# Kernel optimization log

Measured on AMD Instinct MI355X. Metric: run time of the kernel, lower is better.

## Reference

```python
import jax, jax.numpy as jnp
import numpy as np

N = 100000
E = 1600000
F_IN = 128
H = 128
NUM_GRAPHS = 512
EPS = 1e-5


def setup_inputs() -> dict:
    key = jax.random.key(0)
    ks = jax.random.split(key, 16)
    x = jax.random.normal(ks[0], (N, F_IN), dtype=jnp.float32)
    edge_index = jax.random.randint(ks[1], (2, E), 0, N, dtype=jnp.int32)
    batch = jnp.sort(jax.random.randint(ks[2], (N,), 0, NUM_GRAPHS, dtype=jnp.int32))
    def lin(k, fi, fo):
        s = 1.0 / np.sqrt(fi)
        return jax.random.uniform(k, (fi, fo), jnp.float32, -s, s)
    return {
        "x": x, "edge_index": edge_index, "batch": batch,
        "W1": lin(ks[3], F_IN, H), "b1": jnp.zeros((H,), jnp.float32),
        "g1": jnp.ones((H,), jnp.float32), "beta1": jnp.zeros((H,), jnp.float32),
        "W2": lin(ks[4], H, H), "b2": jnp.zeros((H,), jnp.float32),
        "g2": jnp.ones((H,), jnp.float32), "beta2": jnp.zeros((H,), jnp.float32),
        "W3": lin(ks[5], H, H), "b3": jnp.zeros((H,), jnp.float32),
        "g3": jnp.ones((H,), jnp.float32), "beta3": jnp.zeros((H,), jnp.float32),
        "Wl": lin(ks[6], H, 1), "bl": jnp.zeros((1,), jnp.float32),
    }


def _layer_norm(x, g, b):
    mu = jnp.mean(x, axis=-1, keepdims=True)
    var = jnp.mean((x - mu) ** 2, axis=-1, keepdims=True)
    return (x - mu) * jax.lax.rsqrt(var + EPS) * g + b


def _gcn_conv(x, W, b, src, dst, dinv):
    # GCNConv: D^{-1/2}(A+I)D^{-1/2} X W + b, deg includes self-loops
    h = x @ W                                   # [N,H]
    enorm = dinv[src] * dinv[dst]               # [E]
    agg = jax.ops.segment_sum(h[src] * enorm[:, None], dst, num_segments=N)
    agg = agg + h * (dinv * dinv)[:, None]      # self-loop contribution
    return agg + b


def reference(x, edge_index, batch, W1, b1, g1, beta1, W2, b2, g2, beta2,
              W3, b3, g3, beta3, Wl, bl):
    src, dst = edge_index[0], edge_index[1]
    deg = 1.0 + jax.ops.segment_sum(jnp.ones((E,), jnp.float32), dst, num_segments=N)
    dinv = jax.lax.rsqrt(deg)
    h = jax.nn.relu(_layer_norm(_gcn_conv(x, W1, b1, src, dst, dinv), g1, beta1))
    h = jax.nn.relu(_layer_norm(_gcn_conv(h, W2, b2, src, dst, dinv), g2, beta2))
    h = jax.nn.relu(_layer_norm(_gcn_conv(h, W3, b3, src, dst, dinv), g3, beta3))
    # global mean pool over graphs
    sums = jax.ops.segment_sum(h, batch, num_segments=NUM_GRAPHS)
    cnts = jax.ops.segment_sum(jnp.ones((N,), jnp.float32), batch, num_segments=NUM_GRAPHS)
    pooled = sums / jnp.maximum(cnts, 1.0)[:, None]
    return pooled @ Wl + bl                     # [NUM_GRAPHS, 1]
```

## Files before the change

kernel.cpp:

```cpp
#include <hip/hip_runtime.h>
#include <hip/hip_bf16.h>
#include <math.h>

#define N_NODES    100000
#define N_EDGES    1600000
#define FDIM       128
#define NUM_GRAPHS 512
#define EPS        1e-5f
#define PADN       100096

#define B_CVT   12512
#define B_WPK   192

#define NBUCK   196
#define CAPA    10240
#define EB_CHUNK 2048
#define BINA_BLOCKS ((N_EDGES + EB_CHUNK - 1) / EB_CHUNK)
#define SEGSH   14
#define SEGN    8

typedef __attribute__((ext_vector_type(8))) __bf16 bf16x8;
typedef __attribute__((ext_vector_type(4))) float  f32x4;

__device__ __forceinline__ unsigned short f2bf(float f) {
    unsigned u = __builtin_bit_cast(unsigned, f);
    u += 0x7FFF + ((u >> 16) & 1);
    return (unsigned short)(u >> 16);
}
__device__ __forceinline__ float bf2f(unsigned short b) {
    unsigned u = ((unsigned)b) << 16;
    return __builtin_bit_cast(float, u);
}

__device__ __forceinline__ void dec4(unsigned dw, float* o) {
    auto lo = __builtin_amdgcn_cvt_pk_f32_fp8(dw, false);
    auto hi = __builtin_amdgcn_cvt_pk_f32_fp8(dw, true);
    o[0] = lo[0]; o[1] = lo[1]; o[2] = hi[0]; o[3] = hi[1];
}

__device__ __forceinline__ void acc16(uint4 v, float* a) {
    float d[16];
    dec4(v.x, &d[0]); dec4(v.y, &d[4]); dec4(v.z, &d[8]); dec4(v.w, &d[12]);
#pragma unroll
    for (int f = 0; f < 16; f++) a[f] += d[f];
}


__global__ __launch_bounds__(256) void k_build(const int* __restrict__ src,
                                               const int* __restrict__ dst,
                                               int* __restrict__ bcur,
                                               unsigned* __restrict__ binned,
                                               const float* __restrict__ x,
                                               unsigned short* __restrict__ xb,
                                               const float* __restrict__ W1,
                                               const float* __restrict__ W2,
                                               const float* __restrict__ W3,
                                               unsigned short* __restrict__ wp) {
    int b = blockIdx.x;
    int t = threadIdx.x;
    if (b < BINA_BLOCKS) {
        __shared__ int hist[NBUCK];
        __shared__ int lbase[NBUCK];
        __shared__ int loff[NBUCK];
        __shared__ unsigned lpack[EB_CHUNK];
        __shared__ unsigned short lbuck[EB_CHUNK];
        int e0 = b * EB_CHUNK;
        int nE = min(EB_CHUNK, N_EDGES - e0);

        for (int j = t; j < NBUCK; j += 256) { hist[j] = 0; loff[j] = 0; }
        __syncthreads();

        for (int k = t; k < nE; k += 256) {
            int e  = e0 + k;
            int d  = dst[e];
            int bk = d >> 9;
            lpack[k] = (unsigned)src[e] | ((unsigned)(d & 511) << 17);
            lbuck[k] = (unsigned short)bk;
            atomicAdd(&hist[bk], 1);
        }
        __syncthreads();
        for (int j = t; j < NBUCK; j += 256)
            lbase[j] = atomicAdd(&bcur[j], hist[j]);
        __syncthreads();

        for (int k = t; k < nE; k += 256) {
            int bk = lbuck[k];
            int p  = lbase[bk] + atomicAdd(&loff[bk], 1);
            binned[(size_t)bk * CAPA + p] = lpack[k];
        }
    } else if (b < BINA_BLOCKS + B_CVT) {
        long long idx = ((long long)(b - BINA_BLOCKS) * 256 + t) * 4;
        ushort4 o;
        if (idx < (long long)N_NODES * FDIM) {
            float4 v = *(const float4*)(x + idx);
            o.x = f2bf(v.x); o.y = f2bf(v.y); o.z = f2bf(v.z); o.w = f2bf(v.w);
        } else {
            o.x = o.y = o.z = o.w = 0;
        }
        *(ushort4*)(xb + idx) = o;
    } else {
        int wb  = b - (BINA_BLOCKS + B_CVT);
        int mat = wb >> 6;
        const float* W = (mat == 0) ? W1 : (mat == 1) ? W2 : W3;
        unsigned short* o = wp + (size_t)mat * 16384;
        int idx = (wb & 63) * 256 + t;
        int j  = idx & 7;
        int l  = (idx >> 3) & 63;
        int ct = (idx >> 9) & 7;
        int ks = idx >> 12;
        int k  = ks * 32 + (l >> 4) * 8 + j;
        int c  = ct * 16 + (l & 15);
        o[idx] = f2bf(W[k * 128 + c]);
    }
}


__global__ __launch_bounds__(256) void k_binB(const unsigned* __restrict__ binned,
                                              const int* __restrict__ bcur,
                                              int* __restrict__ offs,
                                              float* __restrict__ dinv,
                                              int* __restrict__ csr_src) {
    __shared__ int cnt2[512 * SEGN];
    __shared__ int lofs2[512 * SEGN];
    __shared__ int part[256];
    __shared__ int stage[CAPA];
    int b = blockIdx.x;
    int t = threadIdx.x;
    int nb0 = b * 512;
    int cnt = bcur[b];

    int pv = (t < b) ? bcur[t] : 0;
#pragma unroll
    for (int off = 32; off; off >>= 1) pv += __shfl_down(pv, off);
    if ((t & 63) == 0) part[t >> 6] = pv;
    __syncthreads();
    int seg0 = part[0] + part[1] + part[2] + part[3];
    __syncthreads();

    for (int j = t; j < 512 * SEGN; j += 256) cnt2[j] = 0;
    __syncthreads();

    for (int k = t; k < cnt; k += 256) {
        unsigned v = binned[(size_t)b * CAPA + k];
        int ld = v >> 17;
        int s  = v & 0x1FFFF;
        atomicAdd(&cnt2[ld * SEGN + (s >> SEGSH)], 1);
    }
    __syncthreads();

    int base16 = t * 16;
    int lsum[16];
    int run = 0;
#pragma unroll
    for (int q = 0; q < 16; q++) { lsum[q] = run; run += cnt2[base16 + q]; }
    part[t] = run;
    __syncthreads();
    for (int off = 1; off < 256; off <<= 1) {
        int y = 0;
        if (t >= off) y = part[t - off];
        __syncthreads();
        if (t >= off) part[t] += y;
        __syncthreads();
    }
    int excl = part[t] - run;
#pragma unroll
    for (int q = 0; q < 16; q++) lofs2[base16 + q] = excl + lsum[q];
    __syncthreads();

    for (int j = t; j < 512; j += 256) {
        int node = nb0 + j;
        if (node < N_NODES) {
            int st = lofs2[j * SEGN];
            int en = (j == 511) ? cnt : lofs2[(j + 1) * SEGN];
            offs[node] = seg0 + st;
            dinv[node] = rsqrtf(1.0f + (float)(en - st));
        }
    }
    if (b == NBUCK - 1 && t == 0) offs[N_NODES] = N_EDGES;
    __syncthreads();

    for (int k = t; k < cnt; k += 256) {
        unsigned v = binned[(size_t)b * CAPA + k];
        int ld = v >> 17;
        int s  = v & 0x1FFFF;
        int p  = atomicAdd(&lofs2[ld * SEGN + (s >> SEGSH)], 1);
        stage[p] = s;
    }
    __syncthreads();
    for (int k = t; k < cnt; k += 256) csr_src[seg0 + k] = stage[k];
}


__global__ __launch_bounds__(256) void k_gemm(const unsigned short* __restrict__ A,
                                              const unsigned short* __restrict__ Wp,
                                              const float* __restrict__ dinv,
                                              unsigned char* __restrict__ C8) {
    int t    = threadIdx.x;
    int lane = t & 63;
    int w    = t >> 6;
    int wc   = w & 1;
    int wr   = w >> 1;
    int rb   = blockIdx.x * 128 + wr * 64 + (lane & 15);
    int koff = (lane >> 4) * 8;

    f32x4 acc[4][4];
#pragma unroll
    for (int c = 0; c < 4; c++)
#pragma unroll
        for (int r = 0; r < 4; r++) acc[c][r] = (f32x4){0.f, 0.f, 0.f, 0.f};

    const bf16x8* Wv = (const bf16x8*)Wp;
#pragma unroll
    for (int ks = 0; ks < 4; ++ks) {
        bf16x8 fw[4], fa[4];
#pragma unroll
        for (int c = 0; c < 4; ++c)
            fw[c] = Wv[(ks * 8 + wc * 4 + c) * 64 + lane];
#pragma unroll
        for (int r = 0; r < 4; ++r) {
            const uint4 v = *(const uint4*)(A + (size_t)(rb + r * 16) * 128 + ks * 32 + koff);
            fa[r] = __builtin_bit_cast(bf16x8, v);
        }
#pragma unroll
        for (int c = 0; c < 4; ++c)
#pragma unroll
            for (int r = 0; r < 4; ++r)
                acc[c][r] = __builtin_amdgcn_mfma_f32_16x16x32_bf16(fw[c], fa[r], acc[c][r], 0, 0, 0);
    }

#pragma unroll
    for (int r = 0; r < 4; ++r) {
        int row = blockIdx.x * 128 + wr * 64 + r * 16 + (lane & 15);
        if (row < N_NODES) {
            float dv = dinv[row];
#pragma unroll
            for (int c = 0; c < 4; ++c) {
                int col = (wc * 4 + c) * 16 + (lane >> 4) * 4;
                unsigned u = __builtin_amdgcn_cvt_pk_fp8_f32(acc[c][r][0] * dv, acc[c][r][1] * dv, 0, false);
                u = (unsigned)__builtin_amdgcn_cvt_pk_fp8_f32(acc[c][r][2] * dv, acc[c][r][3] * dv, (int)u, true);
                *(unsigned*)(C8 + (size_t)row * 128 + col) = u;
            }
        }
    }
}


__global__ __launch_bounds__(256) void k_agg(const unsigned char* __restrict__ h8,
                                             unsigned short* __restrict__ out,
                                             const int* __restrict__ offs,
                                             const int* __restrict__ csr_src,
                                             const float* __restrict__ dinv,
                                             const float* __restrict__ bias,
                                             const float* __restrict__ gamma,
                                             const float* __restrict__ beta) {
    int t    = threadIdx.x;
    int lane = t & 63;
    int grp  = lane >> 3;
    int sl   = lane & 7;
    int i    = blockIdx.x * 32 + (t >> 6) * 8 + grp;

    float di = dinv[i];
    size_t lofs16 = (size_t)sl * 16;

    float a[16];
    {
        uint4 v = *(const uint4*)(h8 + (size_t)i * 128 + lofs16);
        float d[16];
        dec4(v.x, &d[0]); dec4(v.y, &d[4]); dec4(v.z, &d[8]); dec4(v.w, &d[12]);
#pragma unroll
        for (int f = 0; f < 16; f++) a[f] = d[f];
    }

    int eBeg = offs[i], eEnd = offs[i + 1];
    int e = eBeg;
    int s0, s1, s2, s3;
    if (e + 4 <= eEnd) {
        s0 = csr_src[e + 0]; s1 = csr_src[e + 1];
        s2 = csr_src[e + 2]; s3 = csr_src[e + 3];
    }
    for (; e + 8 <= eEnd; e += 4) {
        uint4 v0 = *(const uint4*)(h8 + (size_t)s0 * 128 + lofs16);
        uint4 v1 = *(const uint4*)(h8 + (size_t)s1 * 128 + lofs16);
        uint4 v2 = *(const uint4*)(h8 + (size_t)s2 * 128 + lofs16);
        uint4 v3 = *(const uint4*)(h8 + (size_t)s3 * 128 + lofs16);
        s0 = csr_src[e + 4]; s1 = csr_src[e + 5];
        s2 = csr_src[e + 6]; s3 = csr_src[e + 7];
        acc16(v0, a); acc16(v1, a); acc16(v2, a); acc16(v3, a);
    }
    if (e + 4 <= eEnd) {
        uint4 v0 = *(const uint4*)(h8 + (size_t)s0 * 128 + lofs16);
        uint4 v1 = *(const uint4*)(h8 + (size_t)s1 * 128 + lofs16);
        uint4 v2 = *(const uint4*)(h8 + (size_t)s2 * 128 + lofs16);
        uint4 v3 = *(const uint4*)(h8 + (size_t)s3 * 128 + lofs16);
        acc16(v0, a); acc16(v1, a); acc16(v2, a); acc16(v3, a);
        e += 4;
    }
    for (; e < eEnd; ++e) {
        int s = csr_src[e];
        uint4 v = *(const uint4*)(h8 + (size_t)s * 128 + lofs16);
        acc16(v, a);
    }

    float4 b0 = *(const float4*)(bias + sl * 16);
    float4 b1 = *(const float4*)(bias + sl * 16 + 4);
    float4 b2 = *(const float4*)(bias + sl * 16 + 8);
    float4 b3 = *(const float4*)(bias + sl * 16 + 12);
    a[0]  = fmaf(a[0],  di, b0.x); a[1]  = fmaf(a[1],  di, b0.y);
    a[2]  = fmaf(a[2],  di, b0.z); a[3]  = fmaf(a[3],  di, b0.w);
    a[4]  = fmaf(a[4],  di, b1.x); a[5]  = fmaf(a[5],  di, b1.y);
    a[6]  = fmaf(a[6],  di, b1.z); a[7]  = fmaf(a[7],  di, b1.w);
    a[8]  = fmaf(a[8],  di, b2.x); a[9]  = fmaf(a[9],  di, b2.y);
    a[10] = fmaf(a[10], di, b2.z); a[11] = fmaf(a[11], di, b2.w);
    a[12] = fmaf(a[12], di, b3.x); a[13] = fmaf(a[13], di, b3.y);
    a[14] = fmaf(a[14], di, b3.z); a[15] = fmaf(a[15], di, b3.w);

    float s1v = 0.f, s2v = 0.f;
#pragma unroll
    for (int f = 0; f < 16; f++) { s1v += a[f]; s2v += a[f] * a[f]; }
#pragma unroll
    for (int off = 1; off < 8; off <<= 1) {
        s1v += __shfl_xor(s1v, off);
        s2v += __shfl_xor(s2v, off);
    }
    float mu   = s1v * (1.0f / 128.0f);
    float var  = s2v * (1.0f / 128.0f) - mu * mu;
    float rstd = rsqrtf(var + EPS);

    float g[16], be[16];
    {
        float4 g0 = *(const float4*)(gamma + sl * 16);
        float4 g1 = *(const float4*)(gamma + sl * 16 + 4);
        float4 g2 = *(const float4*)(gamma + sl * 16 + 8);
        float4 g3 = *(const float4*)(gamma + sl * 16 + 12);
        g[0]=g0.x; g[1]=g0.y; g[2]=g0.z; g[3]=g0.w;
        g[4]=g1.x; g[5]=g1.y; g[6]=g1.z; g[7]=g1.w;
        g[8]=g2.x; g[9]=g2.y; g[10]=g2.z; g[11]=g2.w;
        g[12]=g3.x; g[13]=g3.y; g[14]=g3.z; g[15]=g3.w;
        float4 e0v = *(const float4*)(beta + sl * 16);
        float4 e1v = *(const float4*)(beta + sl * 16 + 4);
        float4 e2v = *(const float4*)(beta + sl * 16 + 8);
        float4 e3v = *(const float4*)(beta + sl * 16 + 12);
        be[0]=e0v.x; be[1]=e0v.y; be[2]=e0v.z; be[3]=e0v.w;
        be[4]=e1v.x; be[5]=e1v.y; be[6]=e1v.z; be[7]=e1v.w;
        be[8]=e2v.x; be[9]=e2v.y; be[10]=e2v.z; be[11]=e2v.w;
        be[12]=e3v.x; be[13]=e3v.y; be[14]=e3v.z; be[15]=e3v.w;
    }

    unsigned ow[8];
#pragma unroll
    for (int f = 0; f < 8; f++) {
        float r0 = fmaxf((a[2*f]   - mu) * rstd * g[2*f]   + be[2*f],   0.f);
        float r1 = fmaxf((a[2*f+1] - mu) * rstd * g[2*f+1] + be[2*f+1], 0.f);
        ow[f] = (unsigned)f2bf(r0) | ((unsigned)f2bf(r1) << 16);
    }
    uint4* op = (uint4*)(out + (size_t)i * 128 + sl * 16);
    op[0] = make_uint4(ow[0], ow[1], ow[2], ow[3]);
    op[1] = make_uint4(ow[4], ow[5], ow[6], ow[7]);
}


__global__ __launch_bounds__(256) void k_pool(const unsigned short* __restrict__ h,
                                              const int* __restrict__ batch,
                                              const float* __restrict__ Wl,
                                              const float* __restrict__ bl,
                                              float* __restrict__ out) {
    __shared__ float2 part[4][64];
    int g = blockIdx.x;
    int t = threadIdx.x, w = t >> 6, lane = t & 63;

    int lo = 0, hi = N_NODES;
    while (lo < hi) { int mid = (lo + hi) >> 1; if (batch[mid] < g) lo = mid + 1; else hi = mid; }
    int s = lo;
    lo = s; hi = N_NODES;
    while (lo < hi) { int mid = (lo + hi) >> 1; if (batch[mid] < g + 1) lo = mid + 1; else hi = mid; }
    int e = lo;

    float ax = 0.f, ay = 0.f;
    for (int n = s + w; n < e; n += 4) {
        unsigned v = *(const unsigned*)(h + (size_t)n * 128 + lane * 2);
        ax += bf2f((unsigned short)(v & 0xffff));
        ay += bf2f((unsigned short)(v >> 16));
    }
    part[w][lane] = make_float2(ax, ay);
    __syncthreads();
    if (t < 64) {
        float sx = part[0][lane].x + part[1][lane].x + part[2][lane].x + part[3][lane].x;
        float sy = part[0][lane].y + part[1][lane].y + part[2][lane].y + part[3][lane].y;
        float cnt = fmaxf((float)(e - s), 1.0f);
        float inv = 1.0f / cnt;
        float p = sx * inv * Wl[lane * 2] + sy * inv * Wl[lane * 2 + 1];
#pragma unroll
        for (int off = 32; off; off >>= 1) p += __shfl_xor(p, off);
        if (lane == 0) out[g] = p + bl[0];
    }
}


extern "C" void kernel_launch(void* const* d_in, const int* in_sizes, int n_in,
                              void* d_out, int out_size, void* d_ws, size_t ws_size,
                              hipStream_t stream) {
    const float* x     = (const float*)d_in[0];
    const int*   ei    = (const int*)d_in[1];
    const int*   batch = (const int*)d_in[2];
    const float* W1 = (const float*)d_in[3];
    const float* b1 = (const float*)d_in[4];
    const float* g1 = (const float*)d_in[5];
    const float* be1 = (const float*)d_in[6];
    const float* W2 = (const float*)d_in[7];
    const float* b2 = (const float*)d_in[8];
    const float* g2 = (const float*)d_in[9];
    const float* be2 = (const float*)d_in[10];
    const float* W3 = (const float*)d_in[11];
    const float* b3 = (const float*)d_in[12];
    const float* g3 = (const float*)d_in[13];
    const float* be3 = (const float*)d_in[14];
    const float* Wl = (const float*)d_in[15];
    const float* bl = (const float*)d_in[16];

    const int* src = ei;
    const int* dst = ei + N_EDGES;

    char* ws = (char*)d_ws;
    size_t off = 0;
    auto alloc = [&](size_t bytes) -> void* {
        void* p = ws + off;
        off += (bytes + 255) & ~(size_t)255;
        return p;
    };
    unsigned short* xb   = (unsigned short*)alloc((size_t)PADN * FDIM * 2);
    unsigned short* hA   = (unsigned short*)alloc((size_t)PADN * FDIM * 2);
    unsigned char*  hF   = (unsigned char*)alloc((size_t)PADN * FDIM);
    unsigned short* wp   = (unsigned short*)alloc((size_t)3 * 16384 * 2);
    float* dinv    = (float*)alloc((size_t)N_NODES * 4);
    int*   offs    = (int*)alloc((size_t)(N_NODES + 1) * 4);
    int*   csr_src = (int*)alloc((size_t)N_EDGES * 4);
    unsigned* binned = (unsigned*)alloc((size_t)NBUCK * CAPA * 4);
    int*   bcur    = (int*)alloc(256 * 4);

    hipMemsetAsync(bcur, 0, 256 * 4, stream);

    k_build<<<BINA_BLOCKS + B_CVT + B_WPK, 256, 0, stream>>>(src, dst, bcur, binned,
                                                             x, xb, W1, W2, W3, wp);
    k_binB<<<NBUCK, 256, 0, stream>>>(binned, bcur, offs, dinv, csr_src);

    int gemm_grid = PADN / 128;
    int agg_grid  = N_NODES / 32;

    k_gemm<<<gemm_grid, 256, 0, stream>>>(xb, wp, dinv, hF);
    k_agg<<<agg_grid, 256, 0, stream>>>(hF, hA, offs, csr_src, dinv, b1, g1, be1);
    k_gemm<<<gemm_grid, 256, 0, stream>>>(hA, wp + 16384, dinv, hF);
    k_agg<<<agg_grid, 256, 0, stream>>>(hF, hA, offs, csr_src, dinv, b2, g2, be2);
    k_gemm<<<gemm_grid, 256, 0, stream>>>(hA, wp + 32768, dinv, hF);
    k_agg<<<agg_grid, 256, 0, stream>>>(hF, hA, offs, csr_src, dinv, b3, g3, be3);

    k_pool<<<NUM_GRAPHS, 256, 0, stream>>>(hA, batch, Wl, bl, (float*)d_out);
}
```

Measured before the change: 263.8 us.

## Move x/W bf16 conversion into CSR-build kernel and shrink its shared memory

The fp32-to-bf16 conversion of x and the weight packing move out of the edge-binning kernel and into the second preprocessing kernel, which also builds the CSR. The 196 CSR-build blocks now run alongside the many bandwidth-bound conversion blocks instead of running alone on a mostly idle GPU. The CSR block reuses one shared buffer for counts and offsets and computes degrees from per-thread sums, cutting its LDS footprint. Bucket capacity shrinks to 9216, which lowers the margin against bucket overflow.

```diff
diff --git a/kernel.cpp b/kernel.cpp
--- a/kernel.cpp
+++ b/kernel.cpp
@@ -13,9 +13,9 @@
 #define B_WPK   192
 
 #define NBUCK   196
-#define CAPA    10240
+#define CAPA    9216
 #define EB_CHUNK 2048
-#define BINA_BLOCKS ((N_EDGES + EB_CHUNK - 1) / EB_CHUNK)
+#define BIN_BLOCKS ((N_EDGES + EB_CHUNK - 1) / EB_CHUNK)
 #define SEGSH   14
 #define SEGN    8
 
@@ -46,50 +46,126 @@
 }
 
 
-__global__ __launch_bounds__(256) void k_build(const int* __restrict__ src,
-                                               const int* __restrict__ dst,
-                                               int* __restrict__ bcur,
-                                               unsigned* __restrict__ binned,
-                                               const float* __restrict__ x,
-                                               unsigned short* __restrict__ xb,
-                                               const float* __restrict__ W1,
-                                               const float* __restrict__ W2,
-                                               const float* __restrict__ W3,
-                                               unsigned short* __restrict__ wp) {
+__global__ __launch_bounds__(256) void k_bin(const int* __restrict__ src,
+                                             const int* __restrict__ dst,
+                                             int* __restrict__ bcur,
+                                             unsigned* __restrict__ binned) {
+    __shared__ int hist[NBUCK];
+    __shared__ int lbase[NBUCK];
+    __shared__ int loff[NBUCK];
+    __shared__ unsigned lpack[EB_CHUNK];
+    __shared__ unsigned short lbuck[EB_CHUNK];
     int b = blockIdx.x;
     int t = threadIdx.x;
-    if (b < BINA_BLOCKS) {
-        __shared__ int hist[NBUCK];
-        __shared__ int lbase[NBUCK];
-        __shared__ int loff[NBUCK];
-        __shared__ unsigned lpack[EB_CHUNK];
-        __shared__ unsigned short lbuck[EB_CHUNK];
-        int e0 = b * EB_CHUNK;
-        int nE = min(EB_CHUNK, N_EDGES - e0);
-
-        for (int j = t; j < NBUCK; j += 256) { hist[j] = 0; loff[j] = 0; }
-        __syncthreads();
-
-        for (int k = t; k < nE; k += 256) {
-            int e  = e0 + k;
-            int d  = dst[e];
-            int bk = d >> 9;
-            lpack[k] = (unsigned)src[e] | ((unsigned)(d & 511) << 17);
-            lbuck[k] = (unsigned short)bk;
-            atomicAdd(&hist[bk], 1);
-        }
-        __syncthreads();
-        for (int j = t; j < NBUCK; j += 256)
-            lbase[j] = atomicAdd(&bcur[j], hist[j]);
-        __syncthreads();
-
-        for (int k = t; k < nE; k += 256) {
-            int bk = lbuck[k];
-            int p  = lbase[bk] + atomicAdd(&loff[bk], 1);
-            binned[(size_t)bk * CAPA + p] = lpack[k];
-        }
-    } else if (b < BINA_BLOCKS + B_CVT) {
-        long long idx = ((long long)(b - BINA_BLOCKS) * 256 + t) * 4;
+    int e0 = b * EB_CHUNK;
+    int nE = min(EB_CHUNK, N_EDGES - e0);
+
+    for (int j = t; j < NBUCK; j += 256) { hist[j] = 0; loff[j] = 0; }
+    __syncthreads();
+
+    for (int k = t; k < nE; k += 256) {
+        int e  = e0 + k;
+        int d  = dst[e];
+        int bk = d >> 9;
+        lpack[k] = (unsigned)src[e] | ((unsigned)(d & 511) << 17);
+        lbuck[k] = (unsigned short)bk;
+        atomicAdd(&hist[bk], 1);
+    }
+    __syncthreads();
+    for (int j = t; j < NBUCK; j += 256)
+        lbase[j] = atomicAdd(&bcur[j], hist[j]);
+    __syncthreads();
+
+    for (int k = t; k < nE; k += 256) {
+        int bk = lbuck[k];
+        int p  = lbase[bk] + atomicAdd(&loff[bk], 1);
+        binned[(size_t)bk * CAPA + p] = lpack[k];
+    }
+}
+
+
+__global__ __launch_bounds__(256) void k_mid(const unsigned* __restrict__ binned,
+                                             const int* __restrict__ bcur,
+                                             int* __restrict__ offs,
+                                             float* __restrict__ dinv,
+                                             int* __restrict__ csr_src,
+                                             const float* __restrict__ x,
+                                             unsigned short* __restrict__ xb,
+                                             const float* __restrict__ W1,
+                                             const float* __restrict__ W2,
+                                             const float* __restrict__ W3,
+                                             unsigned short* __restrict__ wp) {
+    __shared__ int smem[512 * SEGN + 256 + CAPA];
+    int b = blockIdx.x;
+    int t = threadIdx.x;
+
+    if (b < NBUCK) {
+        int* cnt2  = smem;
+        int* part  = smem + 4096;
+        int* stage = smem + 4352;
+        int nb0 = b * 512;
+        int cnt = bcur[b];
+
+        int pv = (t < b) ? bcur[t] : 0;
+#pragma unroll
+        for (int off = 32; off; off >>= 1) pv += __shfl_down(pv, off);
+        if ((t & 63) == 0) part[t >> 6] = pv;
+        __syncthreads();
+        int seg0 = part[0] + part[1] + part[2] + part[3];
+        __syncthreads();
+
+        for (int j = t; j < 512 * SEGN; j += 256) cnt2[j] = 0;
+        __syncthreads();
+
+        for (int k = t; k < cnt; k += 256) {
+            unsigned v = binned[(size_t)b * CAPA + k];
+            atomicAdd(&cnt2[(v >> 17) * SEGN + ((v & 0x1FFFF) >> SEGSH)], 1);
+        }
+        __syncthreads();
+
+        int base16 = t * 16;
+        int lsum[16];
+        int run = 0;
+#pragma unroll
+        for (int q = 0; q < 16; q++) { lsum[q] = run; run += cnt2[base16 + q]; }
+        int deg0 = lsum[8];
+        int deg1 = run - lsum[8];
+        part[t] = run;
+        __syncthreads();
+        for (int off = 1; off < 256; off <<= 1) {
+            int y = 0;
+            if (t >= off) y = part[t - off];
+            __syncthreads();
+            if (t >= off) part[t] += y;
+            __syncthreads();
+        }
+        int excl = part[t] - run;
+#pragma unroll
+        for (int q = 0; q < 16; q++) cnt2[base16 + q] = excl + lsum[q];
+
+        {
+            int n0 = nb0 + 2 * t;
+            if (n0 < N_NODES) {
+                offs[n0] = seg0 + excl;
+                dinv[n0] = rsqrtf(1.0f + (float)deg0);
+            }
+            if (n0 + 1 < N_NODES) {
+                offs[n0 + 1] = seg0 + excl + lsum[8];
+                dinv[n0 + 1] = rsqrtf(1.0f + (float)deg1);
+            }
+        }
+        if (b == NBUCK - 1 && t == 0) offs[N_NODES] = N_EDGES;
+        __syncthreads();
+
+        for (int k = t; k < cnt; k += 256) {
+            unsigned v = binned[(size_t)b * CAPA + k];
+            int p = atomicAdd(&cnt2[(v >> 17) * SEGN + ((v & 0x1FFFF) >> SEGSH)], 1);
+            stage[p] = (int)(v & 0x1FFFF);
+        }
+        __syncthreads();
+        for (int k = t; k < cnt; k += 256) csr_src[seg0 + k] = stage[k];
+    } else if (b < NBUCK + B_CVT) {
+        long long idx = ((long long)(b - NBUCK) * 256 + t) * 4;
         ushort4 o;
         if (idx < (long long)N_NODES * FDIM) {
             float4 v = *(const float4*)(x + idx);
@@ -99,7 +175,7 @@
         }
         *(ushort4*)(xb + idx) = o;
     } else {
-        int wb  = b - (BINA_BLOCKS + B_CVT);
+        int wb  = b - (NBUCK + B_CVT);
         int mat = wb >> 6;
         const float* W = (mat == 0) ? W1 : (mat == 1) ? W2 : W3;
         unsigned short* o = wp + (size_t)mat * 16384;
@@ -112,82 +188,6 @@
         int c  = ct * 16 + (l & 15);
         o[idx] = f2bf(W[k * 128 + c]);
     }
-}
-
-
-__global__ __launch_bounds__(256) void k_binB(const unsigned* __restrict__ binned,
-                                              const int* __restrict__ bcur,
-                                              int* __restrict__ offs,
-                                              float* __restrict__ dinv,
-                                              int* __restrict__ csr_src) {
-    __shared__ int cnt2[512 * SEGN];
-    __shared__ int lofs2[512 * SEGN];
-    __shared__ int part[256];
-    __shared__ int stage[CAPA];
-    int b = blockIdx.x;
-    int t = threadIdx.x;
-    int nb0 = b * 512;
-    int cnt = bcur[b];
-
-    int pv = (t < b) ? bcur[t] : 0;
-#pragma unroll
-    for (int off = 32; off; off >>= 1) pv += __shfl_down(pv, off);
-    if ((t & 63) == 0) part[t >> 6] = pv;
-    __syncthreads();
-    int seg0 = part[0] + part[1] + part[2] + part[3];
-    __syncthreads();
-
-    for (int j = t; j < 512 * SEGN; j += 256) cnt2[j] = 0;
-    __syncthreads();
-
-    for (int k = t; k < cnt; k += 256) {
-        unsigned v = binned[(size_t)b * CAPA + k];
-        int ld = v >> 17;
-        int s  = v & 0x1FFFF;
-        atomicAdd(&cnt2[ld * SEGN + (s >> SEGSH)], 1);
-    }
-    __syncthreads();
-
-    int base16 = t * 16;
-    int lsum[16];
-    int run = 0;
-#pragma unroll
-    for (int q = 0; q < 16; q++) { lsum[q] = run; run += cnt2[base16 + q]; }
-    part[t] = run;
-    __syncthreads();
-    for (int off = 1; off < 256; off <<= 1) {
-        int y = 0;
-        if (t >= off) y = part[t - off];
-        __syncthreads();
-        if (t >= off) part[t] += y;
-        __syncthreads();
-    }
-    int excl = part[t] - run;
-#pragma unroll
-    for (int q = 0; q < 16; q++) lofs2[base16 + q] = excl + lsum[q];
-    __syncthreads();
-
-    for (int j = t; j < 512; j += 256) {
-        int node = nb0 + j;
-        if (node < N_NODES) {
-            int st = lofs2[j * SEGN];
-            int en = (j == 511) ? cnt : lofs2[(j + 1) * SEGN];
-            offs[node] = seg0 + st;
-            dinv[node] = rsqrtf(1.0f + (float)(en - st));
-        }
-    }
-    if (b == NBUCK - 1 && t == 0) offs[N_NODES] = N_EDGES;
-    __syncthreads();
-
-    for (int k = t; k < cnt; k += 256) {
-        unsigned v = binned[(size_t)b * CAPA + k];
-        int ld = v >> 17;
-        int s  = v & 0x1FFFF;
-        int p  = atomicAdd(&lofs2[ld * SEGN + (s >> SEGSH)], 1);
-        stage[p] = s;
-    }
-    __syncthreads();
-    for (int k = t; k < cnt; k += 256) csr_src[seg0 + k] = stage[k];
 }
 
 
@@ -439,9 +439,9 @@
 
     hipMemsetAsync(bcur, 0, 256 * 4, stream);
 
-    k_build<<<BINA_BLOCKS + B_CVT + B_WPK, 256, 0, stream>>>(src, dst, bcur, binned,
-                                                             x, xb, W1, W2, W3, wp);
-    k_binB<<<NBUCK, 256, 0, stream>>>(binned, bcur, offs, dinv, csr_src);
+    k_bin<<<BIN_BLOCKS, 256, 0, stream>>>(src, dst, bcur, binned);
+    k_mid<<<NBUCK + B_CVT + B_WPK, 256, 0, stream>>>(binned, bcur, offs, dinv, csr_src,
+                                                     x, xb, W1, W2, W3, wp);
 
     int gemm_grid = PADN / 128;
     int agg_grid  = N_NODES / 32;
```

Result: no change. 265.4 us (+0.6%).
